# Performance work log

Hardware: AMD Instinct MI355X
Metric: run time of the kernel (lower is better)

The kernel has to match this reference:

```python
import jax, jax.numpy as jnp
import numpy as np

B, S1, S2 = 8, 2048, 2048
K1_DIM = K2_DIM = 512
PK1_DIM = PK2_DIM = 256
ATT_DIM = 512
DV = 512


def setup_inputs() -> dict:
    key = jax.random.key(0)
    ks = jax.random.split(key, 16)
    s = 0.02
    inp = {
        "k1": jax.random.normal(ks[0], (B, S1, K1_DIM), jnp.float32),
        "k2": jax.random.normal(ks[1], (B, S2, K2_DIM), jnp.float32),
        "preserved_k1": jax.random.normal(ks[2], (B, S1, PK1_DIM), jnp.float32),
        "preserved_k2": jax.random.normal(ks[3], (B, S2, PK2_DIM), jnp.float32),
        "v1": jax.random.normal(ks[4], (B, S1, DV), jnp.float32),
        "v2": jax.random.normal(ks[5], (B, S2, DV), jnp.float32),
        # Linear params stored as [in, out] (x @ W + b == torch Linear)
        "W_k1": jax.random.normal(ks[6], (K1_DIM, ATT_DIM), jnp.float32) * s,
        "b_k1": jnp.zeros((ATT_DIM,), jnp.float32),
        "W_k2": jax.random.normal(ks[7], (K2_DIM, ATT_DIM), jnp.float32) * s,
        "b_k2": jnp.zeros((ATT_DIM,), jnp.float32),
        "W_pk1": jax.random.normal(ks[8], (K1_DIM + PK1_DIM, ATT_DIM), jnp.float32) * s,
        "b_pk1": jnp.zeros((ATT_DIM,), jnp.float32),
        "W_pk2": jax.random.normal(ks[9], (K2_DIM + PK2_DIM, ATT_DIM), jnp.float32) * s,
        "b_pk2": jnp.zeros((ATT_DIM,), jnp.float32),
        # lengths in [S/2, S) so no softmax row is fully masked (original exits on NaN)
        "k1_lengths": jax.random.randint(ks[10], (B,), S1 // 2, S1, jnp.int32).astype(jnp.int64),
        "k2_lengths": jax.random.randint(ks[11], (B,), S2 // 2, S2, jnp.int32).astype(jnp.int64),
    }
    return inp


def _mask(k1_lengths, k2_lengths):
    # Faithful to the original loop: a position is masked iff EXACTLY ONE of
    # (row >= l1) / (col >= l2) holds (mask counter == 1, not >= 1).
    row_over = (jnp.arange(S1)[None, :, None] >= k1_lengths[:, None, None])  # [B,S1,1]
    col_over = (jnp.arange(S2)[None, None, :] >= k2_lengths[:, None, None])  # [B,1,S2]
    return (row_over.astype(jnp.int32) + col_over.astype(jnp.int32)) == 1  # [B,S1,S2]


def reference(k1, k2, preserved_k1, preserved_k2, v1, v2,
              W_k1, b_k1, W_k2, b_k2, W_pk1, b_pk1, W_pk2, b_pk2,
              k1_lengths, k2_lengths):
    pk1 = jnp.concatenate([k1, preserved_k1], axis=-1) @ W_pk1 + b_pk1  # [B,S1,A]
    pk2 = jnp.concatenate([k2, preserved_k2], axis=-1) @ W_pk2 + b_pk2  # [B,S2,A]
    k1p = k1 @ W_k1 + b_k1  # [B,S1,A]
    k2p = k2 @ W_k2 + b_k2  # [B,S2,A]

    score_1 = jnp.einsum("bsa,bta->bst", k1p, pk2)   # [B,S1,S2]
    score_2 = jnp.einsum("bsa,bta->bst", pk1, k2p)   # [B,S1,S2]

    mask = _mask(k1_lengths, k2_lengths)
    score_1 = jnp.where(mask, -jnp.inf, score_1)
    score_2 = jnp.where(mask, -jnp.inf, score_2)

    w1 = jax.nn.softmax(jnp.swapaxes(score_1, 1, 2), axis=-1)  # [B,S2,S1]
    w2 = jax.nn.softmax(score_2, axis=-1)                      # [B,S1,S2]

    o1 = jnp.einsum("bts,bsd->btd", w1, v1)  # [B,S2,DV]
    o2 = jnp.einsum("bst,btd->bsd", w2, v2)  # [B,S1,DV]
    # NOTE: original returns ragged per-sample slices of w1/w2; we return the
    # full padded weight matrices (slice w1[i,:l2,:l1], w2[i,:l1,:l2] to match).
    return (o1, o2, w1, w2)
```

## Files before the change

kernel.cpp:

```cpp
#include <hip/hip_runtime.h>

typedef _Float16 half8 __attribute__((ext_vector_type(8)));
typedef float    floatx4 __attribute__((ext_vector_type(4)));
typedef unsigned short u16;

constexpr int Bn  = 8;
constexpr int Sq  = 2048;
constexpr int KD  = 512;
constexpr int PKD = 256;
constexpr int AD  = 512;
constexpr int DV  = 512;

__device__ __forceinline__ void llds16(const void* g, void* l)
{
    __builtin_amdgcn_global_load_lds(
        (const __attribute__((address_space(1))) unsigned int*)g,
        (__attribute__((address_space(3))) unsigned int*)l, 16, 0, 0);
}

__global__ __launch_bounds__(256)
void transpose_cast_k(const float* __restrict__ in, _Float16* __restrict__ out,
                      int inRows, int inCols, long long bsIn, long long bsOut)
{
    __shared__ float t[32][33];
    const int b = blockIdx.z;
    in  += (long long)b * bsIn;
    out += (long long)b * bsOut;
    const int tx = threadIdx.x & 31;
    const int ty = threadIdx.x >> 5;
    const int c0 = blockIdx.x * 32;
    const int r0 = blockIdx.y * 32;
#pragma unroll
    for (int i = 0; i < 4; ++i)
        t[ty + 8*i][tx] = in[(long long)(r0 + ty + 8*i) * inCols + c0 + tx];
    __syncthreads();
#pragma unroll
    for (int i = 0; i < 4; ++i)
        out[(long long)(c0 + ty + 8*i) * inRows + r0 + tx] = (_Float16)t[tx][ty + 8*i];
}

template<bool A_F32, bool OUT_F16>
__global__ __launch_bounds__(256, 2)
void gemm_k(const void* __restrict__ A1v, const void* __restrict__ A2v, int Ksplit,
            int lda1, int lda2, long long bsA,
            const _Float16* __restrict__ Bm, int ldb, long long bsB,
            void* __restrict__ Cv, int ldc, long long bsC,
            const float* __restrict__ bias, int K)
{
    __shared__ __align__(16) unsigned char AsRaw[A_F32 ? 16384 : 8192];
    __shared__ __align__(16) unsigned char BsRaw[8192];

    const int tid  = threadIdx.x;
    const int lane = tid & 63;
    const int wave = tid >> 6;
    const int wm   = (wave >> 1) * 64;
    const int wn   = (wave & 1) * 64;
    const int fr   = lane & 15;
    const int fq   = lane >> 4;

    const int tm = blockIdx.y, tn = blockIdx.x, bz = blockIdx.z;
    const long long aRowBase = (long long)tm * 128;
    const long long bRowBase = (long long)tn * 128;
    const _Float16* Bbase = Bm + (long long)bz * bsB;

    floatx4 acc[4][4];
#pragma unroll
    for (int i = 0; i < 4; ++i)
#pragma unroll
        for (int j = 0; j < 4; ++j) acc[i][j] = (floatx4)0.0f;

    for (int k0 = 0; k0 < K; k0 += 32) {
        __syncthreads();

        if (A_F32) {
            const float* A1 = (const float*)A1v + (long long)bz * bsA;
            const float* A2 = (const float*)A2v;
#pragma unroll
            for (int is = 0; is < 4; ++is) {
                const int r  = (tid >> 3) + is * 32;
                const int ch = (tid & 7) ^ (r & 7);
                const int kk = k0 + ch * 4;
                const float* src = (kk < Ksplit)
                    ? A1 + (aRowBase + r) * lda1 + kk
                    : A2 + (aRowBase + r) * lda2 + (kk - Ksplit);
                llds16(src, AsRaw + tid * 16 + is * 4096);
            }
        } else {
            const _Float16* A1 = (const _Float16*)A1v + (long long)bz * bsA;
#pragma unroll
            for (int is = 0; is < 2; ++is) {
                const int r  = (tid >> 2) + is * 64;
                const int ch = (tid & 3) ^ (r & 3);
                llds16(A1 + (aRowBase + r) * lda1 + k0 + ch * 8,
                       AsRaw + tid * 16 + is * 4096);
            }
        }
#pragma unroll
        for (int is = 0; is < 2; ++is) {
            const int r  = (tid >> 2) + is * 64;
            const int ch = (tid & 3) ^ (r & 3);
            llds16(Bbase + (bRowBase + r) * ldb + k0 + ch * 8,
                   BsRaw + tid * 16 + is * 4096);
        }

        __syncthreads();

        half8 af[4], bf[4];
        if (A_F32) {
            const float* As32 = (const float*)AsRaw;
#pragma unroll
            for (int i = 0; i < 4; ++i) {
                const int r  = wm + i * 16 + fr;
                const int c0 = ((2 * fq) ^ (r & 7)) * 4;
                const int c1 = ((2 * fq + 1) ^ (r & 7)) * 4;
                floatx4 f0 = *(const floatx4*)(As32 + r * 32 + c0);
                floatx4 f1 = *(const floatx4*)(As32 + r * 32 + c1);
                half8 h;
#pragma unroll
                for (int j = 0; j < 4; ++j) {
                    h[j]     = (_Float16)f0[j];
                    h[4 + j] = (_Float16)f1[j];
                }
                af[i] = h;
            }
        } else {
            const _Float16* As16 = (const _Float16*)AsRaw;
#pragma unroll
            for (int i = 0; i < 4; ++i) {
                const int r  = wm + i * 16 + fr;
                const int ch = fq ^ (r & 3);
                af[i] = *(const half8*)(As16 + r * 32 + ch * 8);
            }
        }
        {
            const _Float16* Bs16 = (const _Float16*)BsRaw;
#pragma unroll
            for (int j = 0; j < 4; ++j) {
                const int r  = wn + j * 16 + fr;
                const int ch = fq ^ (r & 3);
                bf[j] = *(const half8*)(Bs16 + r * 32 + ch * 8);
            }
        }
#pragma unroll
        for (int i = 0; i < 4; ++i)
#pragma unroll
            for (int j = 0; j < 4; ++j)
                acc[i][j] = __builtin_amdgcn_mfma_f32_16x16x32_f16(af[i], bf[j], acc[i][j], 0, 0, 0);
    }

    const int crow0 = tm * 128 + wm + fq * 4;
    const int ccol0 = tn * 128 + wn + fr;
    if (OUT_F16) {
        _Float16* C = (_Float16*)Cv + (long long)bz * bsC;
#pragma unroll
        for (int i = 0; i < 4; ++i)
#pragma unroll
            for (int j = 0; j < 4; ++j) {
                const int col = ccol0 + j * 16;
                const float bv = bias[col];
#pragma unroll
                for (int r = 0; r < 4; ++r)
                    C[(long long)(crow0 + i*16 + r) * ldc + col] = (_Float16)(acc[i][j][r] + bv);
            }
    } else {
        float* C = (float*)Cv + (long long)bz * bsC;
#pragma unroll
        for (int i = 0; i < 4; ++i)
#pragma unroll
            for (int j = 0; j < 4; ++j) {
                const int col = ccol0 + j * 16;
#pragma unroll
                for (int r = 0; r < 4; ++r)
                    C[(long long)(crow0 + i*16 + r) * ldc + col] = acc[i][j][r];
            }
    }
}

__global__ __launch_bounds__(512, 2)
void gemm256_k(const _Float16* __restrict__ Am, long long bsA, int lda,
               const _Float16* __restrict__ Bm, long long bsB, int ldb,
               float* __restrict__ Cm, long long bsC, int ldc, int K)
{
    __shared__ __align__(16) _Float16 lds[65536];

    const int lin0 = (blockIdx.z * 8 + blockIdx.y) * 8 + blockIdx.x;
    const int lin  = (lin0 & 7) * 64 + (lin0 >> 3);
    const int tn   = lin & 7;
    const int tm   = (lin >> 3) & 7;
    const int bz   = lin >> 6;

    const int tid  = threadIdx.x;
    const int lane = tid & 63;
    const int wave = tid >> 6;
    const int wm   = (wave >> 2) * 128;
    const int wn   = (wave & 3) * 64;
    const int fr   = lane & 15;
    const int fq   = lane >> 4;

    const _Float16* Ab = Am + (long long)bz * bsA + (long long)tm * 256 * lda;
    const _Float16* Bb = Bm + (long long)bz * bsB + (long long)tn * 256 * ldb;

    const int sr = lane >> 3;
    const int ch = (lane & 7) ^ sr;
    const _Float16* srcA[2][2];
    const _Float16* srcB[2][2];
#pragma unroll
    for (int h = 0; h < 2; ++h)
#pragma unroll
        for (int l = 0; l < 2; ++l) {
            const int r = h * 128 + (wave * 2 + l) * 8 + sr;
            srcA[h][l] = Ab + (long long)r * lda + ch * 8;
            srcB[h][l] = Bb + (long long)r * ldb + ch * 8;
        }

    auto stageA = [&](int kt, int buf) {
#pragma unroll
        for (int h = 0; h < 2; ++h)
#pragma unroll
            for (int l = 0; l < 2; ++l)
                llds16(srcA[h][l] + kt * 64,
                       lds + buf * 32768 + h * 8192 + (wave * 2 + l) * 512 + lane * 8);
    };
    auto stageB = [&](int kt, int buf) {
#pragma unroll
        for (int h = 0; h < 2; ++h)
#pragma unroll
            for (int l = 0; l < 2; ++l)
                llds16(srcB[h][l] + kt * 64,
                       lds + buf * 32768 + 16384 + h * 8192 + (wave * 2 + l) * 512 + lane * 8);
    };

    auto rdA = [&](int buf, int im, int kk) -> half8 {
        const int row = wm + im * 16 + fr;
        const int c   = (kk * 4 + fq) ^ (row & 7);
        return *(const half8*)(lds + buf * 32768 + row * 64 + c * 8);
    };
    auto rdB = [&](int buf, int jn, int kk) -> half8 {
        const int row = wn + jn * 16 + fr;
        const int c   = (kk * 4 + fq) ^ (row & 7);
        return *(const half8*)(lds + buf * 32768 + 16384 + row * 64 + c * 8);
    };

    floatx4 acc[8][4];
#pragma unroll
    for (int i = 0; i < 8; ++i)
#pragma unroll
        for (int j = 0; j < 4; ++j) acc[i][j] = (floatx4)0.0f;

    const int KT = K >> 6;

    stageA(0, 0);
    stageB(0, 0);
    __syncthreads();

    for (int kt = 0; kt < KT; ++kt) {
        const int buf = kt & 1;
        half8 af[4][2], bf[2][2];
#pragma unroll
        for (int q = 0; q < 4; ++q) {
            const int nh = q >> 1;
            const int mh = (q == 1 || q == 2) ? 1 : 0;
            if (q == 0 || q == 2) {
#pragma unroll
                for (int j = 0; j < 2; ++j)
#pragma unroll
                    for (int kk = 0; kk < 2; ++kk)
                        bf[j][kk] = rdB(buf, nh * 2 + j, kk);
            }
            if (q != 2) {
#pragma unroll
                for (int i = 0; i < 4; ++i)
#pragma unroll
                    for (int kk = 0; kk < 2; ++kk)
                        af[i][kk] = rdA(buf, mh * 4 + i, kk);
            }
            if (kt + 1 < KT) {
                if (q == 0)      stageA(kt + 1, buf ^ 1);
                else if (q == 1) stageB(kt + 1, buf ^ 1);
            }
            __builtin_amdgcn_s_barrier();
            __builtin_amdgcn_s_setprio(1);
#pragma unroll
            for (int i = 0; i < 4; ++i)
#pragma unroll
                for (int j = 0; j < 2; ++j)
#pragma unroll
                    for (int kk = 0; kk < 2; ++kk)
                        acc[mh * 4 + i][nh * 2 + j] =
                            __builtin_amdgcn_mfma_f32_16x16x32_f16(
                                af[i][kk], bf[j][kk], acc[mh * 4 + i][nh * 2 + j], 0, 0, 0);
            __builtin_amdgcn_s_setprio(0);
            if (q < 3) __builtin_amdgcn_s_barrier();
        }
        __syncthreads();
    }

    float* Cb = Cm + (long long)bz * bsC;
    const int crow0 = tm * 256 + wm + fq * 4;
    const int ccol0 = tn * 256 + wn + fr;
#pragma unroll
    for (int i = 0; i < 8; ++i)
#pragma unroll
        for (int j = 0; j < 4; ++j) {
            const long long base = (long long)(crow0 + i * 16) * ldc + ccol0 + j * 16;
#pragma unroll
            for (int r = 0; r < 4; ++r)
                Cb[base + (long long)r * ldc] = acc[i][j][r];
        }
}

__device__ __forceinline__ int load_len(const int* __restrict__ p, int b)
{
    return (p[1] == 0) ? p[2 * b] : p[b];
}

__global__ __launch_bounds__(256)
void softmax_mask_k(float* __restrict__ w, _Float16* __restrict__ wh,
                    const int* __restrict__ lenR, const int* __restrict__ lenC)
{
    const int b = blockIdx.y;
    const int r = blockIdx.x;
    const long long rowOff = ((long long)b * Sq + r) * (long long)Sq;
    float* row = w + rowOff;
    const int lr = load_len(lenR, b);
    const int lc = load_len(lenC, b);
    const bool rover = (r >= lr);
    const int tid  = threadIdx.x;
    const int lane = tid & 63;
    const int wave = tid >> 6;

    floatx4 x0 = *(const floatx4*)(row + tid * 8);
    floatx4 x1 = *(const floatx4*)(row + tid * 8 + 4);
    float v[8];
#pragma unroll
    for (int j = 0; j < 4; ++j) { v[j] = x0[j]; v[4 + j] = x1[j]; }

    float m = -3.0e38f;
#pragma unroll
    for (int j = 0; j < 8; ++j) {
        const int c = tid * 8 + j;
        if (rover != (c >= lc)) v[j] = -__builtin_inff();
        m = fmaxf(m, v[j]);
    }
#pragma unroll
    for (int off = 32; off > 0; off >>= 1) m = fmaxf(m, __shfl_xor(m, off, 64));
    __shared__ float redm[4], reds[4];
    if (lane == 0) redm[wave] = m;
    __syncthreads();
    m = fmaxf(fmaxf(redm[0], redm[1]), fmaxf(redm[2], redm[3]));

    float s = 0.f;
#pragma unroll
    for (int j = 0; j < 8; ++j) { v[j] = __expf(v[j] - m); s += v[j]; }
#pragma unroll
    for (int off = 32; off > 0; off >>= 1) s += __shfl_xor(s, off, 64);
    if (lane == 0) reds[wave] = s;
    __syncthreads();
    s = reds[0] + reds[1] + reds[2] + reds[3];
    const float inv = 1.0f / s;
#pragma unroll
    for (int j = 0; j < 4; ++j) { x0[j] = v[j] * inv; x1[j] = v[4 + j] * inv; }
    *(floatx4*)(row + tid * 8)     = x0;
    *(floatx4*)(row + tid * 8 + 4) = x1;
    if (wh != nullptr) {
        half8 h;
#pragma unroll
        for (int j = 0; j < 4; ++j) { h[j] = (_Float16)x0[j]; h[4 + j] = (_Float16)x1[j]; }
        *(half8*)(wh + rowOff + tid * 8) = h;
    }
}

extern "C" void kernel_launch(void* const* d_in, const int* in_sizes, int n_in,
                              void* d_out, int out_size, void* d_ws, size_t ws_size,
                              hipStream_t stream)
{
    (void)in_sizes; (void)n_in; (void)out_size;
    const float* k1    = (const float*)d_in[0];
    const float* k2    = (const float*)d_in[1];
    const float* pk1in = (const float*)d_in[2];
    const float* pk2in = (const float*)d_in[3];
    const float* v1    = (const float*)d_in[4];
    const float* v2    = (const float*)d_in[5];
    const float* W_k1  = (const float*)d_in[6];
    const float* b_k1  = (const float*)d_in[7];
    const float* W_k2  = (const float*)d_in[8];
    const float* b_k2  = (const float*)d_in[9];
    const float* W_pk1 = (const float*)d_in[10];
    const float* b_pk1 = (const float*)d_in[11];
    const float* W_pk2 = (const float*)d_in[12];
    const float* b_pk2 = (const float*)d_in[13];
    const int* len1 = (const int*)d_in[14];
    const int* len2 = (const int*)d_in[15];

    float* out = (float*)d_out;
    float* o1 = out;
    float* o2 = o1 + (long long)Bn * Sq * DV;
    float* w1 = o2 + (long long)Bn * Sq * DV;
    float* w2 = w1 + (long long)Bn * Sq * Sq;

    _Float16* k1p = (_Float16*)o1;
    _Float16* k2p = k1p + (long long)Bn * Sq * AD;
    _Float16* pk1 = (_Float16*)o2;
    _Float16* pk2 = pk1 + (long long)Bn * Sq * AD;

    _Float16* vT1   = (_Float16*)d_ws;
    _Float16* vT2   = vT1 + (long long)Bn * DV * Sq;
    _Float16* WTk1  = vT2 + (long long)Bn * DV * Sq;
    _Float16* WTk2  = WTk1 + AD * KD;
    _Float16* WTpk1 = WTk2 + AD * KD;
    _Float16* WTpk2 = WTpk1 + AD * (KD + PKD);

    const unsigned long long fixedHalves =
        2ull * Bn * DV * Sq + 2ull * AD * KD + 2ull * AD * (KD + PKD);
    _Float16* w1h = (_Float16*)d_ws + fixedHalves;
    _Float16* w2h = w1h + (long long)Bn * Sq * Sq;
    const bool fast =
        ws_size >= (fixedHalves + 2ull * Bn * Sq * Sq) * sizeof(_Float16);

    transpose_cast_k<<<dim3(AD/32, KD/32, 1), 256, 0, stream>>>(W_k1, WTk1, KD, AD, 0, 0);
    transpose_cast_k<<<dim3(AD/32, KD/32, 1), 256, 0, stream>>>(W_k2, WTk2, KD, AD, 0, 0);
    transpose_cast_k<<<dim3(AD/32, (KD+PKD)/32, 1), 256, 0, stream>>>(W_pk1, WTpk1, KD+PKD, AD, 0, 0);
    transpose_cast_k<<<dim3(AD/32, (KD+PKD)/32, 1), 256, 0, stream>>>(W_pk2, WTpk2, KD+PKD, AD, 0, 0);
    transpose_cast_k<<<dim3(DV/32, Sq/32, Bn), 256, 0, stream>>>(v1, vT1, Sq, DV,
        (long long)Sq*DV, (long long)Sq*DV);
    transpose_cast_k<<<dim3(DV/32, Sq/32, Bn), 256, 0, stream>>>(v2, vT2, Sq, DV,
        (long long)Sq*DV, (long long)Sq*DV);

    const dim3 gProj(AD/128, (Bn*Sq)/128, 1);
    gemm_k<true, true><<<gProj, 256, 0, stream>>>(
        k1, k1, KD, KD, KD, 0,  WTk1, KD, 0,  k1p, AD, 0, b_k1, KD);
    gemm_k<true, true><<<gProj, 256, 0, stream>>>(
        k2, k2, KD, KD, KD, 0,  WTk2, KD, 0,  k2p, AD, 0, b_k2, KD);
    gemm_k<true, true><<<gProj, 256, 0, stream>>>(
        k1, pk1in, KD, KD, PKD, 0,  WTpk1, KD+PKD, 0,  pk1, AD, 0, b_pk1, KD+PKD);
    gemm_k<true, true><<<gProj, 256, 0, stream>>>(
        k2, pk2in, KD, KD, PKD, 0,  WTpk2, KD+PKD, 0,  pk2, AD, 0, b_pk2, KD+PKD);

    const dim3 gScore(Sq/256, Sq/256, Bn);
    gemm256_k<<<gScore, 512, 0, stream>>>(
        pk2, (long long)Sq*AD, AD,
        k1p, (long long)Sq*AD, AD,
        w1, (long long)Sq*Sq, Sq, AD);
    gemm256_k<<<gScore, 512, 0, stream>>>(
        pk1, (long long)Sq*AD, AD,
        k2p, (long long)Sq*AD, AD,
        w2, (long long)Sq*Sq, Sq, AD);

    softmax_mask_k<<<dim3(Sq, Bn), 256, 0, stream>>>(w1, fast ? w1h : nullptr, len2, len1);
    softmax_mask_k<<<dim3(Sq, Bn), 256, 0, stream>>>(w2, fast ? w2h : nullptr, len1, len2);

    const dim3 gOut(DV/128, Sq/128, Bn);
    if (fast) {
        gemm_k<false, false><<<gOut, 256, 0, stream>>>(
            w1h, w1h, 0, Sq, Sq, (long long)Sq*Sq,
            vT1, Sq, (long long)DV*Sq,
            o1, DV, (long long)Sq*DV, nullptr, Sq);
        gemm_k<false, false><<<gOut, 256, 0, stream>>>(
            w2h, w2h, 0, Sq, Sq, (long long)Sq*Sq,
            vT2, Sq, (long long)DV*Sq,
            o2, DV, (long long)Sq*DV, nullptr, Sq);
    } else {
        gemm_k<true, false><<<gOut, 256, 0, stream>>>(
            w1, w1, Sq, Sq, Sq, (long long)Sq*Sq,
            vT1, Sq, (long long)DV*Sq,
            o1, DV, (long long)Sq*DV, nullptr, Sq);
        gemm_k<true, false><<<gOut, 256, 0, stream>>>(
            w2, w2, Sq, Sq, Sq, (long long)Sq*Sq,
            vT2, Sq, (long long)DV*Sq,
            o2, DV, (long long)Sq*DV, nullptr, Sq);
    }
}
```

Before: 906.1 us.

## Add 256x128 fp16 GEMM kernel, pre-cast concatenated inputs, batch paired GEMMs

Adds a 512-thread 256x128-tile fp16 MFMA GEMM with XOR-swizzled LDS, direct global-to-LDS loads and an XCD-aware block remap. It handles two independent problems per launch through a z-split. The projection inputs are first cast and concatenated into fp16 buffers, so the four projection GEMMs become two launches, and the two weight-times-V output GEMMs become one. The aim is to stop re-reading and converting fp32 inputs inside every GEMM and to cut launch count while improving tile efficiency. The cost is an extra cast pass and scratch buffers for the concatenated inputs placed in the output region.

```diff
diff --git a/kernel.cpp b/kernel.cpp
--- a/kernel.cpp
+++ b/kernel.cpp
@@ -39,6 +39,24 @@
         out[(long long)(c0 + ty + 8*i) * inRows + r0 + tx] = (_Float16)t[tx][ty + 8*i];
 }
 
+__global__ __launch_bounds__(256)
+void cast_cat_k(const float* __restrict__ x, const float* __restrict__ y,
+                _Float16* __restrict__ out)
+{
+    const int idx = blockIdx.x * 256 + threadIdx.x;
+    const int e   = idx * 8;
+    const int r   = e / 768;
+    const int c   = e % 768;
+    const float* src = (c < 512) ? (x + (long long)r * 512 + c)
+                                 : (y + (long long)r * 256 + (c - 512));
+    const floatx4 f0 = *(const floatx4*)(src);
+    const floatx4 f1 = *(const floatx4*)(src + 4);
+    half8 h;
+#pragma unroll
+    for (int j = 0; j < 4; ++j) { h[j] = (_Float16)f0[j]; h[4 + j] = (_Float16)f1[j]; }
+    *(half8*)(out + (long long)e) = h;
+}
+
 template<bool A_F32, bool OUT_F16>
 __global__ __launch_bounds__(256, 2)
 void gemm_k(const void* __restrict__ A1v, const void* __restrict__ A2v, int Ksplit,
@@ -307,6 +325,184 @@
             for (int r = 0; r < 4; ++r)
                 Cb[base + (long long)r * ldc] = acc[i][j][r];
         }
+}
+
+template<bool OUT_F16>
+__global__ __launch_bounds__(512, 2)
+void gemm256x128_k(const _Float16* __restrict__ A0, const _Float16* __restrict__ A1,
+                   long long bsA, int lda,
+                   const _Float16* __restrict__ B0, const _Float16* __restrict__ B1,
+                   long long bsB, int ldb,
+                   void* __restrict__ C0, void* __restrict__ C1,
+                   long long bsC, int ldc,
+                   const float* __restrict__ bias0, const float* __restrict__ bias1,
+                   int K, int zsplit)
+{
+    __shared__ __align__(16) _Float16 lds[49152];
+
+    const int gx   = gridDim.x, gy = gridDim.y;
+    const int nwg  = gx * gy * gridDim.z;
+    const int lin0 = (blockIdx.z * gy + blockIdx.y) * gx + blockIdx.x;
+    const int cpx  = nwg >> 3;
+    const int lin  = (lin0 & 7) * cpx + (lin0 >> 3);
+    const int tn   = lin % gx;
+    const int tmp2 = lin / gx;
+    const int tm   = tmp2 % gy;
+    const int bz   = tmp2 / gy;
+
+    const bool sel = (bz >= zsplit);
+    const int  bzl = sel ? (bz - zsplit) : bz;
+    const _Float16* Am = sel ? A1 : A0;
+    const _Float16* Bm = sel ? B1 : B0;
+
+    const int tid  = threadIdx.x;
+    const int lane = tid & 63;
+    const int wave = tid >> 6;
+    const int wm   = (wave >> 2) * 128;
+    const int wn   = (wave & 3) * 32;
+    const int fr   = lane & 15;
+    const int fq   = lane >> 4;
+
+    const _Float16* Ab = Am + (long long)bzl * bsA + (long long)tm * 256 * lda;
+    const _Float16* Bb = Bm + (long long)bzl * bsB + (long long)tn * 128 * ldb;
+
+    const int sr = lane >> 3;
+    const int ch = (lane & 7) ^ sr;
+    const _Float16* srcA[2][2];
+    const _Float16* srcB[2];
+#pragma unroll
+    for (int h = 0; h < 2; ++h)
+#pragma unroll
+        for (int l = 0; l < 2; ++l)
+            srcA[h][l] = Ab + (long long)(h * 128 + (wave * 2 + l) * 8 + sr) * lda + ch * 8;
+#pragma unroll
+    for (int l = 0; l < 2; ++l)
+        srcB[l] = Bb + (long long)((wave * 2 + l) * 8 + sr) * ldb + ch * 8;
+
+    auto stageA = [&](int kt, int buf) {
+#pragma unroll
+        for (int h = 0; h < 2; ++h)
+#pragma unroll
+            for (int l = 0; l < 2; ++l)
+                llds16(srcA[h][l] + kt * 64,
+                       lds + buf * 24576 + h * 8192 + (wave * 2 + l) * 512 + lane * 8);
+    };
+    auto stageB = [&](int kt, int buf) {
+#pragma unroll
+        for (int l = 0; l < 2; ++l)
+            llds16(srcB[l] + kt * 64,
+                   lds + buf * 24576 + 16384 + (wave * 2 + l) * 512 + lane * 8);
+    };
+
+    auto rdA = [&](int buf, int im, int kk) -> half8 {
+        const int row = wm + im * 16 + fr;
+        const int c   = (kk * 4 + fq) ^ (row & 7);
+        return *(const half8*)(lds + buf * 24576 + row * 64 + c * 8);
+    };
+    auto rdB = [&](int buf, int jn, int kk) -> half8 {
+        const int row = wn + jn * 16 + fr;
+        const int c   = (kk * 4 + fq) ^ (row & 7);
+        return *(const half8*)(lds + buf * 24576 + 16384 + row * 64 + c * 8);
+    };
+
+    floatx4 acc[8][2];
+#pragma unroll
+    for (int i = 0; i < 8; ++i)
+#pragma unroll
+        for (int j = 0; j < 2; ++j) acc[i][j] = (floatx4)0.0f;
+
+    const int KT = K >> 6;
+
+    stageA(0, 0);
+    stageB(0, 0);
+    __syncthreads();
+
+    for (int kt = 0; kt < KT; ++kt) {
+        const int buf = kt & 1;
+        half8 afA[4][2], afB[4][2], bf0[2], bf1[2];
+
+#pragma unroll
+        for (int kk = 0; kk < 2; ++kk) bf0[kk] = rdB(buf, 0, kk);
+#pragma unroll
+        for (int i = 0; i < 4; ++i)
+#pragma unroll
+            for (int kk = 0; kk < 2; ++kk) afA[i][kk] = rdA(buf, i, kk);
+        if (kt + 1 < KT) stageA(kt + 1, buf ^ 1);
+        __builtin_amdgcn_s_barrier();
+        __builtin_amdgcn_s_setprio(1);
+#pragma unroll
+        for (int i = 0; i < 4; ++i)
+#pragma unroll
+            for (int kk = 0; kk < 2; ++kk)
+                acc[i][0] = __builtin_amdgcn_mfma_f32_16x16x32_f16(afA[i][kk], bf0[kk], acc[i][0], 0, 0, 0);
+        __builtin_amdgcn_s_setprio(0);
+        __builtin_amdgcn_s_barrier();
+
+#pragma unroll
+        for (int i = 0; i < 4; ++i)
+#pragma unroll
+            for (int kk = 0; kk < 2; ++kk) afB[i][kk] = rdA(buf, 4 + i, kk);
+        if (kt + 1 < KT) stageB(kt + 1, buf ^ 1);
+        __builtin_amdgcn_s_barrier();
+        __builtin_amdgcn_s_setprio(1);
+#pragma unroll
+        for (int i = 0; i < 4; ++i)
+#pragma unroll
+            for (int kk = 0; kk < 2; ++kk)
+                acc[4 + i][0] = __builtin_amdgcn_mfma_f32_16x16x32_f16(afB[i][kk], bf0[kk], acc[4 + i][0], 0, 0, 0);
+        __builtin_amdgcn_s_setprio(0);
+        __builtin_amdgcn_s_barrier();
+
+#pragma unroll
+        for (int kk = 0; kk < 2; ++kk) bf1[kk] = rdB(buf, 1, kk);
+        __builtin_amdgcn_s_barrier();
+        __builtin_amdgcn_s_setprio(1);
+#pragma unroll
+        for (int i = 0; i < 4; ++i)
+#pragma unroll
+            for (int kk = 0; kk < 2; ++kk)
+                acc[4 + i][1] = __builtin_amdgcn_mfma_f32_16x16x32_f16(afB[i][kk], bf1[kk], acc[4 + i][1], 0, 0, 0);
+        __builtin_amdgcn_s_setprio(0);
+        __builtin_amdgcn_s_barrier();
+
+        __builtin_amdgcn_s_setprio(1);
+#pragma unroll
+        for (int i = 0; i < 4; ++i)
+#pragma unroll
+            for (int kk = 0; kk < 2; ++kk)
+                acc[i][1] = __builtin_amdgcn_mfma_f32_16x16x32_f16(afA[i][kk], bf1[kk], acc[i][1], 0, 0, 0);
+        __builtin_amdgcn_s_setprio(0);
+
+        __syncthreads();
+    }
+
+    const int crow0 = tm * 256 + wm + fq * 4;
+    const int ccol0 = tn * 128 + wn + fr;
+    if (OUT_F16) {
+        const float* bias = sel ? bias1 : bias0;
+        _Float16* C = (_Float16*)(sel ? C1 : C0) + (long long)bzl * bsC;
+#pragma unroll
+        for (int i = 0; i < 8; ++i)
+#pragma unroll
+            for (int j = 0; j < 2; ++j) {
+                const int col = ccol0 + j * 16;
+                const float bv = bias[col];
+#pragma unroll
+                for (int r = 0; r < 4; ++r)
+                    C[(long long)(crow0 + i * 16 + r) * ldc + col] = (_Float16)(acc[i][j][r] + bv);
+            }
+    } else {
+        float* C = (float*)(sel ? C1 : C0) + (long long)bzl * bsC;
+#pragma unroll
+        for (int i = 0; i < 8; ++i)
+#pragma unroll
+            for (int j = 0; j < 2; ++j) {
+                const int col = ccol0 + j * 16;
+#pragma unroll
+                for (int r = 0; r < 4; ++r)
+                    C[(long long)(crow0 + i * 16 + r) * ldc + col] = acc[i][j][r];
+            }
+    }
 }
 
 __device__ __forceinline__ int load_len(const int* __restrict__ p, int b)
@@ -402,6 +598,8 @@
     _Float16* k2p = k1p + (long long)Bn * Sq * AD;
     _Float16* pk1 = (_Float16*)o2;
     _Float16* pk2 = pk1 + (long long)Bn * Sq * AD;
+    _Float16* cat1 = pk2 + (long long)Bn * Sq * AD;
+    _Float16* cat2 = cat1 + (long long)Bn * Sq * (KD + PKD);
 
     _Float16* vT1   = (_Float16*)d_ws;
     _Float16* vT2   = vT1 + (long long)Bn * DV * Sq;
@@ -425,16 +623,19 @@
         (long long)Sq*DV, (long long)Sq*DV);
     transpose_cast_k<<<dim3(DV/32, Sq/32, Bn), 256, 0, stream>>>(v2, vT2, Sq, DV,
         (long long)Sq*DV, (long long)Sq*DV);
-
-    const dim3 gProj(AD/128, (Bn*Sq)/128, 1);
-    gemm_k<true, true><<<gProj, 256, 0, stream>>>(
-        k1, k1, KD, KD, KD, 0,  WTk1, KD, 0,  k1p, AD, 0, b_k1, KD);
-    gemm_k<true, true><<<gProj, 256, 0, stream>>>(
-        k2, k2, KD, KD, KD, 0,  WTk2, KD, 0,  k2p, AD, 0, b_k2, KD);
-    gemm_k<true, true><<<gProj, 256, 0, stream>>>(
-        k1, pk1in, KD, KD, PKD, 0,  WTpk1, KD+PKD, 0,  pk1, AD, 0, b_pk1, KD+PKD);
-    gemm_k<true, true><<<gProj, 256, 0, stream>>>(
-        k2, pk2in, KD, KD, PKD, 0,  WTpk2, KD+PKD, 0,  pk2, AD, 0, b_pk2, KD+PKD);
+    cast_cat_k<<<dim3((Bn*Sq*(KD+PKD))/(256*8), 1, 1), 256, 0, stream>>>(k1, pk1in, cat1);
+    cast_cat_k<<<dim3((Bn*Sq*(KD+PKD))/(256*8), 1, 1), 256, 0, stream>>>(k2, pk2in, cat2);
+
+    gemm256x128_k<true><<<dim3(AD/128, (Bn*Sq)/256, 2), 512, 0, stream>>>(
+        cat1, cat2, 0, KD+PKD,
+        WTk1, WTk2, 0, KD,
+        k1p, k2p, 0, AD,
+        b_k1, b_k2, KD, 1);
+    gemm256x128_k<true><<<dim3(AD/128, (Bn*Sq)/256, 2), 512, 0, stream>>>(
+        cat1, cat2, 0, KD+PKD,
+        WTpk1, WTpk2, 0, KD+PKD,
+        pk1, pk2, 0, AD,
+        b_pk1, b_pk2, KD+PKD, 1);
 
     const dim3 gScore(Sq/256, Sq/256, Bn);
     gemm256_k<<<gScore, 512, 0, stream>>>(
@@ -449,17 +650,14 @@
     softmax_mask_k<<<dim3(Sq, Bn), 256, 0, stream>>>(w1, fast ? w1h : nullptr, len2, len1);
     softmax_mask_k<<<dim3(Sq, Bn), 256, 0, stream>>>(w2, fast ? w2h : nullptr, len1, len2);
 
-    const dim3 gOut(DV/128, Sq/128, Bn);
     if (fast) {
-        gemm_k<false, false><<<gOut, 256, 0, stream>>>(
-            w1h, w1h, 0, Sq, Sq, (long long)Sq*Sq,
-            vT1, Sq, (long long)DV*Sq,
-            o1, DV, (long long)Sq*DV, nullptr, Sq);
-        gemm_k<false, false><<<gOut, 256, 0, stream>>>(
-            w2h, w2h, 0, Sq, Sq, (long long)Sq*Sq,
-            vT2, Sq, (long long)DV*Sq,
-            o2, DV, (long long)Sq*DV, nullptr, Sq);
+        gemm256x128_k<false><<<dim3(DV/128, Sq/256, 2*Bn), 512, 0, stream>>>(
+            w1h, w2h, (long long)Sq*Sq, Sq,
+            vT1, vT2, (long long)DV*Sq, Sq,
+            o1, o2, (long long)Sq*DV, DV,
+            nullptr, nullptr, Sq, Bn);
     } else {
+        const dim3 gOut(DV/128, Sq/128, Bn);
         gemm_k<true, false><<<gOut, 256, 0, stream>>>(
             w1, w1, Sq, Sq, Sq, (long long)Sq*Sq,
             vT1, Sq, (long long)DV*Sq,
```

Measured after the change: 854.1 us. 5.7% less time.
